# Kernel tuning notes

Measured on AMD Instinct MI355X. Metric: run time of the kernel, lower is better.

The kernel has to match this reference:

```python
import jax, jax.numpy as jnp
import numpy as np

B, T, N, C = 4, 12, 200, 64
ATT = 128      # hard-coded attention_dim in GCN_OPERATION
H = 64         # AdjGen LSTM hidden size
DA = 64        # AdjGen adjacency projection dim
OUT_F = 128    # num_of_out_features
PRED = 12      # predict_length
NFILT = 3      # len(filters) per STSGCM
DATA_LEN = T - 4  # after 2 STSGCL layers


def setup_inputs() -> dict:
    key = jax.random.key(0)
    ks = jax.random.split(key, 16)
    s = 0.05
    f32 = jnp.float32
    return {
        "x": jax.random.normal(ks[0], (B, T, N, C), f32),
        "cur_epi": 5,
        "his_hn": jax.random.normal(ks[1], (B, H), f32),
        "his_cn": jax.random.normal(ks[2], (B, H), f32),
        "Wqkv": jax.random.normal(ks[3], (C, 3 * ATT), f32) * s,
        "bqkv": jnp.zeros((3 * ATT,), f32),
        "Wlin": jax.random.normal(ks[4], (ATT, C), f32) * s,
        "blin": jnp.zeros((C,), f32),
        "Wa": jax.random.normal(ks[5], (C, DA), f32) * s,
        "Wb": jax.random.normal(ks[6], (C, DA), f32) * s,
        "Wx_lstm": jax.random.normal(ks[7], (C, 4 * H), f32) * s,
        "Wh_lstm": jax.random.normal(ks[8], (H, 4 * H), f32) * s,
        "b_lstm": jnp.zeros((4 * H,), f32),
        "temb0": jax.random.normal(ks[9], (1, T, 1, C), f32) * 0.01,
        "temb1": jax.random.normal(ks[10], (1, T - 2, 1, C), f32) * 0.01,
        "semb": jax.random.normal(ks[11], (1, 1, N, C), f32) * 0.01,
        "Wo": jax.random.normal(ks[12], (DATA_LEN * C, OUT_F), f32) * s,
        "bo": jnp.zeros((OUT_F,), f32),
    }


def _forward(x, his_hn, his_cn, Wqkv, bqkv, Wlin, blin, Wa, Wb,
             Wx_lstm, Wh_lstm, b_lstm, temb0, temb1, semb, Wo, bo):
    dt = x.dtype
    att_scale = jnp.sqrt(jnp.asarray(float(ATT), dt))
    adj_scale = jnp.sqrt(jnp.asarray(float(DA), dt))

    def adjgen(xw):
        # xw: (B, nw, M, C). Stand-in for AdjGen (source unavailable):
        # content-dependent learned adjacency over M=3N nodes + one LSTM step.
        node = xw.mean(axis=(0, 1))                                  # (M, C)
        logits = (node @ Wa) @ (node @ Wb).T / adj_scale             # (M, M)
        adj = jax.nn.sigmoid(logits)
        pooled = xw.mean(axis=(1, 2))                                # (B, C)
        gates = pooled @ Wx_lstm + his_hn @ Wh_lstm + b_lstm
        i, f, g, o = jnp.split(gates, 4, axis=-1)
        c_n = jax.nn.sigmoid(f) * his_cn + jax.nn.sigmoid(i) * jnp.tanh(g)
        h_n = jax.nn.sigmoid(o) * jnp.tanh(c_n)
        return adj, logits, h_n, c_n

    def gcn_op(xw, adj):
        # QK^T softmax attention rescaled by adj, renormalized, then AV.
        Bn, nw, M, Cc = xw.shape
        xf = xw.reshape(Bn * nw, M, Cc)
        qkv = xf @ Wqkv + bqkv
        q, k, v = jnp.split(qkv, 3, axis=-1)                          # (BW, M, ATT)
        scores = jnp.einsum('bmd,bnd->bmn', q, k) / att_scale         # (BW, M, M)
        aw = jax.nn.softmax(scores, axis=-1) * adj
        ssum = aw.sum(-1, keepdims=True)
        mask = (ssum > 0).astype(dt)
        w = aw / (ssum + 1e-8) * mask
        out = jnp.einsum('bmn,bnd->bmd', w, jax.nn.relu(v)) @ Wlin + blin
        return out.reshape(Bn, nw, M, -1)

    def stsgcm(xw, Nn):
        cands = []
        cur = xw
        hn = cn = None
        for _ in range(NFILT):
            adj, _logits, hn, cn = adjgen(cur)
            cur = gcn_op(cur, adj)
            Bn, nw, M, F = cur.shape
            # keep only the middle-window copy of the N vertices: [2N:3N]
            cands.append(cur.reshape(Bn * nw, M, F)[:, 2 * Nn:3 * Nn, :])
        out = jnp.max(jnp.stack(cands, axis=0), axis=0)               # (B*nw, N, F)
        return out, hn, cn

    def stsgcl(xw, temb):
        Bn, Tt, Nn, Cc = xw.shape
        xw = xw + temb + semb                                         # position embedding
        nw = Tt - 2
        idx = jnp.arange(nw)[:, None] + jnp.arange(3)[None, :]        # (nw, 3)
        t_all = xw[:, idx].reshape(Bn, nw, 3 * Nn, Cc)
        out, hn, cn = stsgcm(t_all, Nn)
        return out.reshape(Bn, nw, Nn, -1), hn, cn

    h, hn, cn = stsgcl(x, temb0)
    h, hn, cn = stsgcl(h, temb1)
    # OUTPUT layer: (B, T', N, F) -> (B, N, T'*F) -> ReLU(Linear) -> tile PRED times on dim 1
    Bn, Tt, Nn, F = h.shape
    d = h.transpose(0, 2, 1, 3).reshape(Bn, Nn, Tt * F)
    o1 = jax.nn.relu(d @ Wo + bo)                                     # (B, N, OUT_F)
    return jnp.tile(o1, (1, PRED, 1))                                 # (B, PRED*N, OUT_F)


def reference(x, cur_epi, his_hn, his_cn, Wqkv, bqkv, Wlin, blin, Wa, Wb,
              Wx_lstm, Wh_lstm, b_lstm, temb0, temb1, semb, Wo, bo):
    del cur_epi  # annealing schedule of the (unavailable) AdjGen; unused here
    return _forward(x, his_hn, his_cn, Wqkv, bqkv, Wlin, blin, Wa, Wb,
                    Wx_lstm, Wh_lstm, b_lstm, temb0, temb1, semb, Wo, bo)
```

## Files before the change

### kernel.cpp

```cpp
#include <hip/hip_runtime.h>
#include <hip/hip_bf16.h>
#include <math.h>

constexpr int Bc   = 4;
constexpr int Nc   = 200;
constexpr int Cc   = 64;
constexpr int Mc   = 600;
constexpr int ATTc = 128;
constexpr int OUTFc = 128;
constexpr int PREDc = 12;
constexpr int MAXBW = 40;
constexpr int MPAD  = 640;

typedef short short4v __attribute__((ext_vector_type(4)));
typedef short short8 __attribute__((ext_vector_type(8)));
typedef float f32x4  __attribute__((ext_vector_type(4)));

static __device__ __forceinline__ void bsplit(float v, short& h, short& l) {
    __hip_bfloat16 hb = __float2bfloat16(v);
    float hf = __bfloat162float(hb);
    __hip_bfloat16 lb = __float2bfloat16(v - hf);
    h = *(short*)&hb; l = *(short*)&lb;
}

__global__ __launch_bounds__(256)
void embed_window_k(const float* __restrict__ src, const float* __restrict__ temb,
                    const float* __restrict__ semb, float* __restrict__ dst,
                    int Tin, int nw, long total)
{
    long idx = (long)blockIdx.x * 256 + threadIdx.x;
    if (idx >= total) return;
    int c = (int)(idx & 63);
    long r = idx >> 6;
    int n = (int)(r % Nc); r /= Nc;
    int j = (int)(r % 3);  r /= 3;
    int w = (int)(r % nw);
    int b = (int)(r / nw);
    int t = w + j;
    dst[idx] = src[(((long)b * Tin + t) * Nc + n) * Cc + c]
             + temb[t * Cc + c] + semb[n * Cc + c];
}

__global__ __launch_bounds__(256)
void mean_nab_k(const float* __restrict__ cur, const float* __restrict__ Wa,
                const float* __restrict__ Wb,
                ushort* __restrict__ NAH, ushort* __restrict__ NAL,
                ushort* __restrict__ NBH, ushort* __restrict__ NBL, int BW)
{
    __shared__ float Ns[64][17];
    __shared__ float Ws[64][132];
    const int m0 = blockIdx.x * 16;
    const int t = threadIdx.x;
    for (int e = t; e < 1024; e += 256) {
        int r = e >> 4, c4 = (e & 15) << 2;
        *(float4*)&Ws[r][c4]      = *(const float4*)&Wa[r * 64 + c4];
        *(float4*)&Ws[r][64 + c4] = *(const float4*)&Wb[r * 64 + c4];
    }
    {
        int row = t >> 4, c4 = (t & 15) << 2;
        int gm = m0 + row;
        float4 sv = make_float4(0.f, 0.f, 0.f, 0.f);
        if (gm < Mc) {
            for (int bw = 0; bw < BW; bw++) {
                const float4 v = *(const float4*)&cur[((long)bw * Mc + gm) * Cc + c4];
                sv.x += v.x; sv.y += v.y; sv.z += v.z; sv.w += v.w;
            }
        }
        const float inv = 1.f / BW;
        Ns[c4 + 0][row] = sv.x * inv; Ns[c4 + 1][row] = sv.y * inv;
        Ns[c4 + 2][row] = sv.z * inv; Ns[c4 + 3][row] = sv.w * inv;
    }
    __syncthreads();
    const int row = t >> 4, c8 = (t & 15) * 8;
    float acc[8] = {};
    for (int k = 0; k < 64; k++) {
        float a = Ns[k][row];
        float b[8];
        *(float4*)&b[0] = *(const float4*)&Ws[k][c8];
        *(float4*)&b[4] = *(const float4*)&Ws[k][c8 + 4];
#pragma unroll
        for (int j = 0; j < 8; j++) acc[j] += a * b[j];
    }
    int gm = m0 + row;
    if (gm < Mc) {
#pragma unroll
        for (int j = 0; j < 8; j++) {
            int col = c8 + j;
            short h, l;
            bsplit(acc[j], h, l);
            if (col < 64) { NAH[gm * 64 + col] = (ushort)h; NAL[gm * 64 + col] = (ushort)l; }
            else { NBH[gm * 64 + col - 64] = (ushort)h; NBL[gm * 64 + col - 64] = (ushort)l; }
        }
    }
}

__global__ __launch_bounds__(256)
void adjmm_k(const ushort* __restrict__ Ah, const ushort* __restrict__ Al,
             const ushort* __restrict__ Bh, const ushort* __restrict__ Bl,
             float* __restrict__ ADJ)
{
    __shared__ __align__(16) ushort As[2][128][40];
    __shared__ __align__(16) ushort Bs[2][128][40];
    const int m0 = blockIdx.y * 128, n0 = blockIdx.x * 128;
    const int t = threadIdx.x;
    const int lane = t & 63, w = t >> 6;
    const int wm = (w >> 1) * 64, wn = (w & 1) * 64;
    const int lm = lane & 15, lq = lane >> 4;

    f32x4 acc[4][4];
#pragma unroll
    for (int i = 0; i < 4; i++)
#pragma unroll
        for (int j = 0; j < 4; j++)
#pragma unroll
            for (int r = 0; r < 4; r++) acc[i][j][r] = 0.f;

    for (int k0 = 0; k0 < 64; k0 += 32) {
        __syncthreads();
#pragma unroll
        for (int p = 0; p < 2; p++) {
            int e = t + p * 256;
            int row = e >> 2, ks = (e & 3) << 3;
            {
                int gm = m0 + row;
                short8 vh, vl;
#pragma unroll
                for (int q = 0; q < 8; q++) { vh[q] = 0; vl[q] = 0; }
                if (gm < Mc) {
                    vh = *(const short8*)(Ah + (long)gm * 64 + k0 + ks);
                    vl = *(const short8*)(Al + (long)gm * 64 + k0 + ks);
                }
                *(short8*)&As[0][row][ks] = vh;
                *(short8*)&As[1][row][ks] = vl;
            }
            {
                int gn = n0 + row;
                short8 vh, vl;
#pragma unroll
                for (int q = 0; q < 8; q++) { vh[q] = 0; vl[q] = 0; }
                if (gn < Mc) {
                    vh = *(const short8*)(Bh + (long)gn * 64 + k0 + ks);
                    vl = *(const short8*)(Bl + (long)gn * 64 + k0 + ks);
                }
                *(short8*)&Bs[0][row][ks] = vh;
                *(short8*)&Bs[1][row][ks] = vl;
            }
        }
        __syncthreads();

        short8 af[4][2], bf[4][2];
#pragma unroll
        for (int i = 0; i < 4; i++) {
            af[i][0] = *(const short8*)&As[0][wm + i * 16 + lm][lq * 8];
            af[i][1] = *(const short8*)&As[1][wm + i * 16 + lm][lq * 8];
        }
#pragma unroll
        for (int j = 0; j < 4; j++) {
            bf[j][0] = *(const short8*)&Bs[0][wn + j * 16 + lm][lq * 8];
            bf[j][1] = *(const short8*)&Bs[1][wn + j * 16 + lm][lq * 8];
        }
#pragma unroll
        for (int i = 0; i < 4; i++)
#pragma unroll
            for (int j = 0; j < 4; j++) {
                acc[i][j] = __builtin_amdgcn_mfma_f32_16x16x32_bf16(af[i][0], bf[j][0], acc[i][j], 0, 0, 0);
                acc[i][j] = __builtin_amdgcn_mfma_f32_16x16x32_bf16(af[i][0], bf[j][1], acc[i][j], 0, 0, 0);
                acc[i][j] = __builtin_amdgcn_mfma_f32_16x16x32_bf16(af[i][1], bf[j][0], acc[i][j], 0, 0, 0);
            }
    }
#pragma unroll
    for (int i = 0; i < 4; i++) {
        int gmb = m0 + wm + i * 16 + lq * 4;
#pragma unroll
        for (int j = 0; j < 4; j++) {
            int gn = n0 + wn + j * 16 + lm;
            if (gn >= Mc) continue;
#pragma unroll
            for (int r = 0; r < 4; r++) {
                int gm = gmb + r;
                if (gm < Mc)
                    ADJ[(long)gm * Mc + gn] = 1.f / (1.f + __expf(-acc[i][j][r] * 0.125f));
            }
        }
    }
}

__global__ __launch_bounds__(256)
void wqkv_prep_k(const float* __restrict__ Wqkv,
                 ushort* __restrict__ WQH, ushort* __restrict__ WQL)
{
    int i = blockIdx.x * 256 + threadIdx.x;
    if (i >= 384 * 64) return;
    int n = i >> 6, c = i & 63;
    short h, l;
    bsplit(Wqkv[c * 384 + n], h, l);
    WQH[n * 64 + c] = (ushort)h;
    WQL[n * 64 + c] = (ushort)l;
}

__global__ __launch_bounds__(256)
void qkv_mfma_k(const float* __restrict__ CURp,
                const ushort* __restrict__ WQH, const ushort* __restrict__ WQL,
                const float* __restrict__ bias,
                ushort* __restrict__ QH, ushort* __restrict__ QL,
                ushort* __restrict__ KH, ushort* __restrict__ KL,
                ushort* __restrict__ VTH, ushort* __restrict__ VTL)
{
    __shared__ __align__(16) ushort SM[36864];
    ushort* AsH = SM;
    ushort* AsL = SM + 9216;
    ushort* BsH = SM + 18432;
    ushort* BsL = SM + 27648;
    const int bid = blockIdx.x;
    const int xcd = bid & 7, slot = bid >> 3;
    const int z = (slot / 15) * 8 + xcd;
    const int r15 = slot % 15;
    const int which = r15 % 3;
    const int m0 = (r15 / 3) * 128;
    const int nb = which * 128;
    const float* A = CURp + (long)z * Mc * Cc;
    const int t = threadIdx.x;
    const int lane = t & 63, w = t >> 6;
    const int wm = (w >> 1) * 64, wn = (w & 1) * 64;
    const int lm = lane & 15, lq = lane >> 4;

#pragma unroll
    for (int p = 0; p < 8; p++) {
        int e = t + p * 256;
        int row = e >> 4, k4 = (e & 15) * 4;
        int gm = m0 + row;
        float4 v = make_float4(0.f, 0.f, 0.f, 0.f);
        if (gm < Mc) v = *(const float4*)(A + (long)gm * 64 + k4);
        short4v h4, l4;
        short hs, ls;
        bsplit(v.x, hs, ls); h4[0] = hs; l4[0] = ls;
        bsplit(v.y, hs, ls); h4[1] = hs; l4[1] = ls;
        bsplit(v.z, hs, ls); h4[2] = hs; l4[2] = ls;
        bsplit(v.w, hs, ls); h4[3] = hs; l4[3] = ls;
        *(short4v*)(AsH + row * 72 + k4) = h4;
        *(short4v*)(AsL + row * 72 + k4) = l4;
    }
#pragma unroll
    for (int p = 0; p < 4; p++) {
        int e = t + p * 256;
        int row = e >> 3, seg = (e & 7) * 8;
        *(short8*)(BsH + row * 72 + seg) = *(const short8*)(WQH + (long)(nb + row) * 64 + seg);
        *(short8*)(BsL + row * 72 + seg) = *(const short8*)(WQL + (long)(nb + row) * 64 + seg);
    }
    __syncthreads();

    f32x4 acc[4][4];
#pragma unroll
    for (int i = 0; i < 4; i++)
#pragma unroll
        for (int j = 0; j < 4; j++)
#pragma unroll
            for (int r = 0; r < 4; r++) acc[i][j][r] = 0.f;

#pragma unroll
    for (int ks = 0; ks < 2; ks++) {
        short8 af[4][2], bf[4][2];
#pragma unroll
        for (int i = 0; i < 4; i++) {
            af[i][0] = *(const short8*)(AsH + (wm + i * 16 + lm) * 72 + ks * 32 + lq * 8);
            af[i][1] = *(const short8*)(AsL + (wm + i * 16 + lm) * 72 + ks * 32 + lq * 8);
        }
#pragma unroll
        for (int j = 0; j < 4; j++) {
            bf[j][0] = *(const short8*)(BsH + (wn + j * 16 + lm) * 72 + ks * 32 + lq * 8);
            bf[j][1] = *(const short8*)(BsL + (wn + j * 16 + lm) * 72 + ks * 32 + lq * 8);
        }
#pragma unroll
        for (int i = 0; i < 4; i++)
#pragma unroll
            for (int j = 0; j < 4; j++) {
                acc[i][j] = __builtin_amdgcn_mfma_f32_16x16x32_bf16(af[i][0], bf[j][0], acc[i][j], 0, 0, 0);
                acc[i][j] = __builtin_amdgcn_mfma_f32_16x16x32_bf16(af[i][0], bf[j][1], acc[i][j], 0, 0, 0);
                acc[i][j] = __builtin_amdgcn_mfma_f32_16x16x32_bf16(af[i][1], bf[j][0], acc[i][j], 0, 0, 0);
            }
    }
    __syncthreads();

    uint* CP = (uint*)SM;
#pragma unroll
    for (int i = 0; i < 4; i++)
#pragma unroll
        for (int j = 0; j < 4; j++) {
            int col = wn + j * 16 + lm;
            float b = bias[nb + col];
#pragma unroll
            for (int r = 0; r < 4; r++) {
                int row = wm + i * 16 + lq * 4 + r;
                float v = acc[i][j][r] + b;
                if (which == 2) v = fmaxf(v, 0.f);
                short hs, ls;
                bsplit(v, hs, ls);
                CP[row * 132 + col] = ((uint)(ushort)ls << 16) | (uint)(ushort)hs;
            }
        }
    __syncthreads();

    if (which == 2) {
        ushort* vh = VTH + (long)z * ATTc * MPAD;
        ushort* vl = VTL + (long)z * ATTc * MPAD;
#pragma unroll
        for (int p = 0; p < 8; p++) {
            int e = t + p * 256;
            int col = e >> 4, rg = (e & 15) * 8;
            if (m0 + rg < Mc) {
                short8 h8, l8;
#pragma unroll
                for (int q = 0; q < 8; q++) {
                    uint u = CP[(rg + q) * 132 + col];
                    h8[q] = (short)(u & 0xffff);
                    l8[q] = (short)(u >> 16);
                }
                *(short8*)(vh + (long)col * MPAD + m0 + rg) = h8;
                *(short8*)(vl + (long)col * MPAD + m0 + rg) = l8;
            }
        }
    } else {
        ushort* dh = (which == 0 ? QH : KH) + (long)z * Mc * ATTc;
        ushort* dl = (which == 0 ? QL : KL) + (long)z * Mc * ATTc;
#pragma unroll
        for (int p = 0; p < 8; p++) {
            int e = t + p * 256;
            int row = e >> 4, seg = (e & 15) * 8;
            int gm = m0 + row;
            if (gm < Mc) {
                short8 h8, l8;
#pragma unroll
                for (int q = 0; q < 8; q++) {
                    uint u = CP[row * 132 + seg + q];
                    h8[q] = (short)(u & 0xffff);
                    l8[q] = (short)(u >> 16);
                }
                *(short8*)(dh + (long)gm * ATTc + seg) = h8;
                *(short8*)(dl + (long)gm * ATTc + seg) = l8;
            }
        }
    }
}

#define ISSUE_K(Dh, Dl, kc_, g_)                                        \
  _Pragma("unroll")                                                     \
  for (int p = 0; p < 4; p++) {                                         \
    int key = (kc_) + srow0 + 32 * p;                                   \
    short8 vh, vl;                                                      \
    _Pragma("unroll")                                                   \
    for (int q2 = 0; q2 < 8; q2++) { vh[q2] = 0; vl[q2] = 0; }          \
    if (key < Mc) {                                                     \
      vh = *(const short8*)(Khz + (long)key * ATTc + (g_) * 64 + sks);  \
      vl = *(const short8*)(Klz + (long)key * ATTc + (g_) * 64 + sks);  \
    }                                                                   \
    Dh[p] = vh; Dl[p] = vl;                                             \
  }

#define ISSUE_V(Dh, Dl, kc_, g_)                                                   \
  _Pragma("unroll")                                                                \
  for (int p = 0; p < 4; p++) {                                                    \
    int att = srow0 + 32 * p;                                                      \
    Dh[p] = *(const short8*)(Vhz + (long)att * MPAD + (kc_) + (g_) * 64 + sks);    \
    Dl[p] = *(const short8*)(Vlz + (long)att * MPAD + (kc_) + (g_) * 64 + sks);    \
  }

#define WRITE_SB(Dh, Dl)                                                \
  _Pragma("unroll")                                                     \
  for (int p = 0; p < 4; p++) {                                         \
    *(short8*)&SB[0][srow0 + 32 * p][sks] = Dh[p];                      \
    *(short8*)&SB[1][srow0 + 32 * p][sks] = Dl[p];                      \
  }

#define MFMA_QK(base_)                                                   \
  _Pragma("unroll")                                                      \
  for (int kk = 0; kk < 2; kk++) {                                       \
    _Pragma("unroll")                                                    \
    for (int j = 0; j < 8; j++) {                                        \
      short8 bh = *(const short8*)&SB[0][j * 16 + lm][kk * 32 + lq * 8]; \
      short8 bl = *(const short8*)&SB[1][j * 16 + lm][kk * 32 + lq * 8]; \
      sacc[j] = __builtin_amdgcn_mfma_f32_16x16x32_bf16(qh[(base_) + kk], bh, sacc[j], 0, 0, 0); \
      sacc[j] = __builtin_amdgcn_mfma_f32_16x16x32_bf16(qh[(base_) + kk], bl, sacc[j], 0, 0, 0); \
      sacc[j] = __builtin_amdgcn_mfma_f32_16x16x32_bf16(ql[(base_) + kk], bh, sacc[j], 0, 0, 0); \
    }                                                                    \
  }

#define MFMA_PV(g_)                                                      \
  _Pragma("unroll")                                                      \
  for (int kk = 0; kk < 2; kk++) {                                       \
    int po = ((g_) * 64 + kk * 32 + lq * 8) ^ ((lm >> 2) << 3);          \
    short8 ph = *(const short8*)&PH[w][lm][po];                          \
    short8 pl = *(const short8*)&PL[w][lm][po];                          \
    _Pragma("unroll")                                                    \
    for (int j = 0; j < 8; j++) {                                        \
      short8 vh = *(const short8*)&SB[0][j * 16 + lm][kk * 32 + lq * 8]; \
      short8 vl = *(const short8*)&SB[1][j * 16 + lm][kk * 32 + lq * 8]; \
      oacc[j] = __builtin_amdgcn_mfma_f32_16x16x32_bf16(ph, vh, oacc[j], 0, 0, 0); \
      oacc[j] = __builtin_amdgcn_mfma_f32_16x16x32_bf16(ph, vl, oacc[j], 0, 0, 0); \
      oacc[j] = __builtin_amdgcn_mfma_f32_16x16x32_bf16(pl, vh, oacc[j], 0, 0, 0); \
    }                                                                    \
  }

__global__ __launch_bounds__(256, 2)
void attn_k(const ushort* __restrict__ QH, const ushort* __restrict__ QL,
            const ushort* __restrict__ KH, const ushort* __restrict__ KL,
            const ushort* __restrict__ VTH, const ushort* __restrict__ VTL,
            const float* __restrict__ adj, uint* __restrict__ OB, float scale)
{
    __shared__ __align__(16) ushort SB[2][128][72];
    __shared__ __align__(16) ushort PH[4][16][152];
    __shared__ __align__(16) ushort PL[4][16][152];
    const int bid = blockIdx.x;
    const int xcd = bid & 7, slot = bid >> 3;
    const int z = (slot / 10) * 8 + xcd;
    const int m0 = (slot % 10) * 64;
    const int t = threadIdx.x;
    const int lane = t & 63, w = t >> 6;
    const int lm = lane & 15, lq = lane >> 4;
    const int qrow0 = m0 + w * 16;
    const int srow0 = t >> 3;
    const int sks   = (t & 7) << 3;

    const ushort* Qhz = QH + (long)z * Mc * ATTc;
    const ushort* Qlz = QL + (long)z * Mc * ATTc;
    const ushort* Khz = KH + (long)z * Mc * ATTc;
    const ushort* Klz = KL + (long)z * Mc * ATTc;
    const ushort* Vhz = VTH + (long)z * ATTc * MPAD;
    const ushort* Vlz = VTL + (long)z * ATTc * MPAD;

    short8 RAh[4], RAl[4], RBh[4], RBl[4];
    ISSUE_K(RAh, RAl, 0, 0);

    short8 qh[4], ql[4];
    {
        int qr = qrow0 + lm;
        if (qr < Mc) {
            const ushort* qp = Qhz + (long)qr * ATTc;
            const ushort* qp2 = Qlz + (long)qr * ATTc;
#pragma unroll
            for (int ks = 0; ks < 4; ks++) {
                qh[ks] = *(const short8*)(qp + ks * 32 + lq * 8);
                ql[ks] = *(const short8*)(qp2 + ks * 32 + lq * 8);
            }
        } else {
#pragma unroll
            for (int ks = 0; ks < 4; ks++)
#pragma unroll
                for (int q = 0; q < 8; q++) { qh[ks][q] = 0; ql[ks][q] = 0; }
        }
    }

    f32x4 oacc[8];
#pragma unroll
    for (int j = 0; j < 8; j++)
#pragma unroll
        for (int r = 0; r < 4; r++) oacc[j][r] = 0.f;
    float Er[4] = {}, Sr[4] = {};
    float adjv[8][4];

    for (int c = 0; c < 5; c++) {
        const int kc = c * 128;
        f32x4 sacc[8];
#pragma unroll
        for (int j = 0; j < 8; j++)
#pragma unroll
            for (int r = 0; r < 4; r++) sacc[j][r] = 0.f;

        __syncthreads();
        WRITE_SB(RAh, RAl);
        ISSUE_K(RBh, RBl, kc, 1);
#pragma unroll
        for (int j = 0; j < 8; j++) {
            int col = kc + j * 16 + lm;
#pragma unroll
            for (int r = 0; r < 4; r++) {
                int row = qrow0 + lq * 4 + r;
                adjv[j][r] = (col < Mc && row < Mc) ? adj[(long)row * Mc + col] : 0.f;
            }
        }
        __syncthreads();
        MFMA_QK(0);

        __syncthreads();
        WRITE_SB(RBh, RBl);
        ISSUE_V(RAh, RAl, kc, 0);
        __syncthreads();
        MFMA_QK(2);

#pragma unroll
        for (int j = 0; j < 8; j++) {
            int col = kc + j * 16 + lm;
            bool cok = col < Mc;
#pragma unroll
            for (int r = 0; r < 4; r++) {
                float e = cok ? __expf(sacc[j][r] * scale) : 0.f;
                float p = e * adjv[j][r];
                Er[r] += e; Sr[r] += p;
                short hs, ls;
                bsplit(p, hs, ls);
                int cs = (j * 16 + lm) ^ (lq << 3);
                PH[w][lq * 4 + r][cs] = (ushort)hs;
                PL[w][lq * 4 + r][cs] = (ushort)ls;
            }
        }

        __syncthreads();
        WRITE_SB(RAh, RAl);
        ISSUE_V(RBh, RBl, kc, 1);
        __syncthreads();
        MFMA_PV(0);

        __syncthreads();
        WRITE_SB(RBh, RBl);
        if (c < 4) { ISSUE_K(RAh, RAl, kc + 128, 0); }
        __syncthreads();
        MFMA_PV(1);
    }

#pragma unroll
    for (int mk = 1; mk <= 8; mk <<= 1)
#pragma unroll
        for (int r = 0; r < 4; r++) {
            Er[r] += __shfl_xor(Er[r], mk, 64);
            Sr[r] += __shfl_xor(Sr[r], mk, 64);
        }
    float inv[4];
#pragma unroll
    for (int r = 0; r < 4; r++) inv[r] = 1.f / (Sr[r] + 1e-8f * Er[r]);
    uint* Oz = OB + (long)z * Mc * ATTc;
#pragma unroll
    for (int j = 0; j < 8; j++)
#pragma unroll
        for (int r = 0; r < 4; r++) {
            int row = qrow0 + lq * 4 + r;
            if (row < Mc) {
                float v = oacc[j][r] * inv[r];
                short hs, ls;
                bsplit(v, hs, ls);
                Oz[(long)row * ATTc + j * 16 + lm] =
                    ((uint)(ushort)ls << 16) | (uint)(ushort)hs;
            }
        }
}

#undef ISSUE_K
#undef ISSUE_V
#undef WRITE_SB
#undef MFMA_QK
#undef MFMA_PV

__global__ __launch_bounds__(256)
void wlin_prep_k(const float* __restrict__ Wlin,
                 ushort* __restrict__ WTH, ushort* __restrict__ WTL)
{
    int i = blockIdx.x * 256 + threadIdx.x;
    if (i >= 64 * 128) return;
    int c = i >> 7, a = i & 127;
    short h, l;
    bsplit(Wlin[a * 64 + c], h, l);
    WTH[c * 128 + a] = (ushort)h;
    WTL[c * 128 + a] = (ushort)l;
}

__global__ __launch_bounds__(256)
void wlin_k(const uint* __restrict__ OB, const ushort* __restrict__ WTH,
            const ushort* __restrict__ WTL, const float* __restrict__ blin,
            float* __restrict__ CUR, int Mtot)
{
    __shared__ __align__(16) ushort As[2][128][40];
    __shared__ __align__(16) ushort Bs[2][64][136];
    const int m0 = blockIdx.x * 128;
    const int t = threadIdx.x;
    const int lane = t & 63, w = t >> 6;
    const int wm = (w >> 1) * 64, wn = (w & 1) * 32;
    const int lm = lane & 15, lq = lane >> 4;

#pragma unroll
    for (int p = 0; p < 4; p++) {
        int e = t + p * 256;
        int row = e >> 4, seg = (e & 15) << 3;
        *(short8*)&Bs[0][row][seg] = *(const short8*)(WTH + row * 128 + seg);
        *(short8*)&Bs[1][row][seg] = *(const short8*)(WTL + row * 128 + seg);
    }

    f32x4 acc[4][2];
#pragma unroll
    for (int i = 0; i < 4; i++)
#pragma unroll
        for (int j = 0; j < 2; j++)
#pragma unroll
            for (int r = 0; r < 4; r++) acc[i][j][r] = 0.f;

    for (int k0 = 0; k0 < 128; k0 += 32) {
        __syncthreads();
#pragma unroll
        for (int p = 0; p < 2; p++) {
            int e = t + p * 256;
            int row = e >> 2, seg = (e & 3) << 3;
            int gm = m0 + row;
            short8 vh, vl;
#pragma unroll
            for (int q = 0; q < 8; q++) { vh[q] = 0; vl[q] = 0; }
            if (gm < Mtot) {
                const uint4 u0 = *(const uint4*)(OB + (long)gm * 128 + k0 + seg);
                const uint4 u1 = *(const uint4*)(OB + (long)gm * 128 + k0 + seg + 4);
#pragma unroll
                for (int q = 0; q < 4; q++) {
                    uint u = ((const uint*)&u0)[q];
                    vh[q] = (short)(u & 0xffff); vl[q] = (short)(u >> 16);
                }
#pragma unroll
                for (int q = 0; q < 4; q++) {
                    uint u = ((const uint*)&u1)[q];
                    vh[4 + q] = (short)(u & 0xffff); vl[4 + q] = (short)(u >> 16);
                }
            }
            *(short8*)&As[0][row][seg] = vh;
            *(short8*)&As[1][row][seg] = vl;
        }
        __syncthreads();

        short8 af[4][2], bf[2][2];
#pragma unroll
        for (int i = 0; i < 4; i++) {
            af[i][0] = *(const short8*)&As[0][wm + i * 16 + lm][lq * 8];
            af[i][1] = *(const short8*)&As[1][wm + i * 16 + lm][lq * 8];
        }
#pragma unroll
        for (int j = 0; j < 2; j++) {
            bf[j][0] = *(const short8*)&Bs[0][wn + j * 16 + lm][k0 + lq * 8];
            bf[j][1] = *(const short8*)&Bs[1][wn + j * 16 + lm][k0 + lq * 8];
        }
#pragma unroll
        for (int i = 0; i < 4; i++)
#pragma unroll
            for (int j = 0; j < 2; j++) {
                acc[i][j] = __builtin_amdgcn_mfma_f32_16x16x32_bf16(af[i][0], bf[j][0], acc[i][j], 0, 0, 0);
                acc[i][j] = __builtin_amdgcn_mfma_f32_16x16x32_bf16(af[i][0], bf[j][1], acc[i][j], 0, 0, 0);
                acc[i][j] = __builtin_amdgcn_mfma_f32_16x16x32_bf16(af[i][1], bf[j][0], acc[i][j], 0, 0, 0);
            }
    }
#pragma unroll
    for (int i = 0; i < 4; i++) {
        int gmb = m0 + wm + i * 16 + lq * 4;
#pragma unroll
        for (int j = 0; j < 2; j++) {
            int col = wn + j * 16 + lm;
            float b = blin[col];
#pragma unroll
            for (int r = 0; r < 4; r++) {
                int gm = gmb + r;
                if (gm < Mtot) CUR[(long)gm * 64 + col] = acc[i][j][r] + b;
            }
        }
    }
}

__global__ __launch_bounds__(256)
void cand_update_k(const float* __restrict__ cur, float* __restrict__ cand,
                   int bw0, long total, int first)
{
    long idx = (long)blockIdx.x * 256 + threadIdx.x;
    if (idx >= total) return;
    int c = (int)(idx & 63);
    long r = idx >> 6;
    int n = (int)(r % Nc);
    int i = (int)(r / Nc);
    long bw = bw0 + i;
    float v = cur[((bw * Mc) + 2 * Nc + n) * Cc + c];
    long o = ((bw * Nc) + n) * Cc + c;
    cand[o] = first ? v : fmaxf(cand[o], v);
}

__global__ __launch_bounds__(128)
void output_k(const float* __restrict__ h2, const float* __restrict__ Wo,
              const float* __restrict__ bo, float* __restrict__ out)
{
    __shared__ float ds[512];
    int row = blockIdx.x;
    int b = row / Nc, n = row % Nc;
    int t = threadIdx.x;
    for (int e = t; e < 512; e += 128) {
        int tt = e >> 6, c = e & 63;
        ds[e] = h2[(((long)b * 8 + tt) * Nc + n) * Cc + c];
    }
    __syncthreads();
    float acc = bo[t];
    for (int e = 0; e < 512; e++) acc += ds[e] * Wo[e * OUTFc + t];
    acc = fmaxf(acc, 0.f);
    for (int p = 0; p < PREDc; p++)
        out[(((long)b * PREDc + p) * Nc + n) * (long)OUTFc + t] = acc;
}

extern "C" void kernel_launch(void* const* d_in, const int* in_sizes, int n_in,
                              void* d_out, int out_size, void* d_ws, size_t ws_size,
                              hipStream_t stream)
{
    (void)in_sizes; (void)n_in; (void)out_size; (void)ws_size;
    const float* x     = (const float*)d_in[0];
    const float* Wqkv  = (const float*)d_in[4];
    const float* bqkv  = (const float*)d_in[5];
    const float* Wlin  = (const float*)d_in[6];
    const float* blin  = (const float*)d_in[7];
    const float* Wa    = (const float*)d_in[8];
    const float* Wb    = (const float*)d_in[9];
    const float* temb0 = (const float*)d_in[13];
    const float* temb1 = (const float*)d_in[14];
    const float* semb  = (const float*)d_in[15];
    const float* Wo    = (const float*)d_in[16];
    const float* bo    = (const float*)d_in[17];
    float* out = (float*)d_out;

    float* ws   = (float*)d_ws;
    float* CUR  = ws;
    float* ADJ  = CUR + (long)MAXBW * Mc * Cc;
    float* CAND = ADJ + (long)Mc * Mc;
    uint*  OB   = (uint*)(CAND + (long)MAXBW * Nc * Cc);
    float* QHf  = (float*)(OB + (long)MAXBW * Mc * ATTc);
    const long QSZ = (long)MAXBW * Mc * ATTc / 2;
    float* QLf  = QHf + QSZ;
    float* KHf  = QLf + QSZ;
    float* KLf  = KHf + QSZ;
    float* VTHf = KLf + QSZ;
    float* VTLf = VTHf + (long)MAXBW * ATTc * MPAD / 2;
    ushort* NAH = (ushort*)(VTLf + (long)MAXBW * ATTc * MPAD / 2);
    ushort* NAL = NAH + Mc * Cc;
    ushort* NBH = NAL + Mc * Cc;
    ushort* NBL = NBH + Mc * Cc;
    ushort* WTH = NBL + Mc * Cc;
    ushort* WTL = WTH + 64 * 128;
    ushort* WQH = WTL + 64 * 128;
    ushort* WQL = WQH + 384 * 64;

    ushort* QH  = (ushort*)QHf;
    ushort* QL  = (ushort*)QLf;
    ushort* KH  = (ushort*)KHf;
    ushort* KL  = (ushort*)KLf;
    ushort* VTH = (ushort*)VTHf;
    ushort* VTL = (ushort*)VTLf;

    const float inv_sqrt_att = 0.08838834764831845f;

    wlin_prep_k<<<dim3(32), dim3(256), 0, stream>>>(Wlin, WTH, WTL);
    wqkv_prep_k<<<dim3(96), dim3(256), 0, stream>>>(Wqkv, WQH, WQL);

    for (int layer = 0; layer < 2; layer++) {
        int Tin = layer ? 10 : 12;
        int nw  = Tin - 2;
        int BW  = Bc * nw;
        int Mtot = BW * Mc;
        const float* src  = layer ? CAND : x;
        const float* temb = layer ? temb1 : temb0;

        long etotal = (long)BW * Mc * Cc;
        embed_window_k<<<dim3((unsigned)((etotal + 255) / 256)), dim3(256), 0, stream>>>(
            src, temb, semb, CUR, Tin, nw, etotal);

        for (int it = 0; it < 3; it++) {
            mean_nab_k<<<dim3(38), dim3(256), 0, stream>>>(
                CUR, Wa, Wb, NAH, NAL, NBH, NBL, BW);
            adjmm_k<<<dim3(5, 5), dim3(256), 0, stream>>>(
                NAH, NAL, NBH, NBL, ADJ);

            qkv_mfma_k<<<dim3(BW * 15), dim3(256), 0, stream>>>(
                CUR, WQH, WQL, bqkv, QH, QL, KH, KL, VTH, VTL);

            attn_k<<<dim3(BW * 10), dim3(256), 0, stream>>>(
                QH, QL, KH, KL, VTH, VTL, ADJ, OB, inv_sqrt_att);

            wlin_k<<<dim3((Mtot + 127) / 128), dim3(256), 0, stream>>>(
                OB, WTH, WTL, blin, CUR, Mtot);

            long mtot = (long)BW * Nc * Cc;
            cand_update_k<<<dim3((unsigned)((mtot + 255) / 256)), dim3(256), 0, stream>>>(
                CUR, CAND, 0, mtot, it == 0 ? 1 : 0);
        }
    }
    output_k<<<dim3(Bc * Nc), dim3(128), 0, stream>>>(CAND, Wo, bo, out);
}
```

Baseline: 753.0 us.

## Use 32x32 MFMA tiles in attention and fuse candidate max into wlin

Moves the attention kernel from 16x16x32 to 32x32x16 bf16 MFMA instructions. Each wave now owns a 32-query by 64-key/attn quadrant, which cuts LDS operand reads per flop. A shared-memory reduction combines the softmax row sums across the two key-half waves. It also folds the per-iteration candidate max update into the wlin epilogue, removing a separate kernel launch and one re-read of CUR. The trade-offs are higher register pressure from the 16-wide accumulators and an extra block barrier.

```diff
diff --git a/kernel.cpp b/kernel.cpp
--- a/kernel.cpp
+++ b/kernel.cpp
@@ -15,6 +15,7 @@
 typedef short short4v __attribute__((ext_vector_type(4)));
 typedef short short8 __attribute__((ext_vector_type(8)));
 typedef float f32x4  __attribute__((ext_vector_type(4)));
+typedef float f32x16 __attribute__((ext_vector_type(16)));
 
 static __device__ __forceinline__ void bsplit(float v, short& h, short& l) {
     __hip_bfloat16 hb = __float2bfloat16(v);
@@ -371,33 +372,35 @@
     *(short8*)&SB[1][srow0 + 32 * p][sks] = Dl[p];                      \
   }
 
-#define MFMA_QK(base_)                                                   \
-  _Pragma("unroll")                                                      \
-  for (int kk = 0; kk < 2; kk++) {                                       \
-    _Pragma("unroll")                                                    \
-    for (int j = 0; j < 8; j++) {                                        \
-      short8 bh = *(const short8*)&SB[0][j * 16 + lm][kk * 32 + lq * 8]; \
-      short8 bl = *(const short8*)&SB[1][j * 16 + lm][kk * 32 + lq * 8]; \
-      sacc[j] = __builtin_amdgcn_mfma_f32_16x16x32_bf16(qh[(base_) + kk], bh, sacc[j], 0, 0, 0); \
-      sacc[j] = __builtin_amdgcn_mfma_f32_16x16x32_bf16(qh[(base_) + kk], bl, sacc[j], 0, 0, 0); \
-      sacc[j] = __builtin_amdgcn_mfma_f32_16x16x32_bf16(ql[(base_) + kk], bh, sacc[j], 0, 0, 0); \
-    }                                                                    \
+#define MFMA32(a, b, c) __builtin_amdgcn_mfma_f32_32x32x16_bf16(a, b, c, 0, 0, 0)
+
+#define QK_ROUND(g_)                                                       \
+  _Pragma("unroll")                                                        \
+  for (int al = 0; al < 4; al++) {                                         \
+    short8 b0h = *(const short8*)&SB[0][kh64 + l31][al * 16 + lh8];        \
+    short8 b0l = *(const short8*)&SB[1][kh64 + l31][al * 16 + lh8];        \
+    short8 b1h = *(const short8*)&SB[0][kh64 + 32 + l31][al * 16 + lh8];   \
+    short8 b1l = *(const short8*)&SB[1][kh64 + 32 + l31][al * 16 + lh8];   \
+    s0 = MFMA32(qh[(g_) * 4 + al], b0h, s0);                               \
+    s1 = MFMA32(qh[(g_) * 4 + al], b1h, s1);                               \
+    s0 = MFMA32(qh[(g_) * 4 + al], b0l, s0);                               \
+    s1 = MFMA32(qh[(g_) * 4 + al], b1l, s1);                               \
+    s0 = MFMA32(ql[(g_) * 4 + al], b0h, s0);                               \
+    s1 = MFMA32(ql[(g_) * 4 + al], b1h, s1);                               \
   }
 
-#define MFMA_PV(g_)                                                      \
-  _Pragma("unroll")                                                      \
-  for (int kk = 0; kk < 2; kk++) {                                       \
-    int po = ((g_) * 64 + kk * 32 + lq * 8) ^ ((lm >> 2) << 3);          \
-    short8 ph = *(const short8*)&PH[w][lm][po];                          \
-    short8 pl = *(const short8*)&PL[w][lm][po];                          \
-    _Pragma("unroll")                                                    \
-    for (int j = 0; j < 8; j++) {                                        \
-      short8 vh = *(const short8*)&SB[0][j * 16 + lm][kk * 32 + lq * 8]; \
-      short8 vl = *(const short8*)&SB[1][j * 16 + lm][kk * 32 + lq * 8]; \
-      oacc[j] = __builtin_amdgcn_mfma_f32_16x16x32_bf16(ph, vh, oacc[j], 0, 0, 0); \
-      oacc[j] = __builtin_amdgcn_mfma_f32_16x16x32_bf16(ph, vl, oacc[j], 0, 0, 0); \
-      oacc[j] = __builtin_amdgcn_mfma_f32_16x16x32_bf16(pl, vh, oacc[j], 0, 0, 0); \
-    }                                                                    \
+#define PV_ROUND(g_)                                                       \
+  _Pragma("unroll")                                                        \
+  for (int kp = 0; kp < 4; kp++) {                                         \
+    short8 pA = *(const short8*)&PHs[qt32 + l31][(g_) * 64 + kp * 16 + lh8]; \
+    short8 pB = *(const short8*)&PLs[qt32 + l31][(g_) * 64 + kp * 16 + lh8]; \
+    short8 v0h = *(const short8*)&SB[0][kh64 + l31][kp * 16 + lh8];        \
+    short8 v0l = *(const short8*)&SB[1][kh64 + l31][kp * 16 + lh8];        \
+    short8 v1h = *(const short8*)&SB[0][kh64 + 32 + l31][kp * 16 + lh8];   \
+    short8 v1l = *(const short8*)&SB[1][kh64 + 32 + l31][kp * 16 + lh8];   \
+    o0 = MFMA32(pA, v0h, o0); o1 = MFMA32(pA, v1h, o1);                    \
+    o0 = MFMA32(pA, v0l, o0); o1 = MFMA32(pA, v1l, o1);                    \
+    o0 = MFMA32(pB, v0h, o0); o1 = MFMA32(pB, v1h, o1);                    \
   }
 
 __global__ __launch_bounds__(256, 2)
@@ -407,16 +410,19 @@
             const float* __restrict__ adj, uint* __restrict__ OB, float scale)
 {
     __shared__ __align__(16) ushort SB[2][128][72];
-    __shared__ __align__(16) ushort PH[4][16][152];
-    __shared__ __align__(16) ushort PL[4][16][152];
+    __shared__ __align__(16) ushort PHs[64][136];
+    __shared__ __align__(16) ushort PLs[64][136];
+    __shared__ float REDs[2][2][2][16];
+    __shared__ float REDe[2][2][2][16];
     const int bid = blockIdx.x;
     const int xcd = bid & 7, slot = bid >> 3;
     const int z = (slot / 10) * 8 + xcd;
     const int m0 = (slot % 10) * 64;
     const int t = threadIdx.x;
     const int lane = t & 63, w = t >> 6;
-    const int lm = lane & 15, lq = lane >> 4;
-    const int qrow0 = m0 + w * 16;
+    const int l31 = lane & 31, lh = lane >> 5, lh8 = lh * 8;
+    const int qt = w & 1, kh = w >> 1;
+    const int qt32 = qt * 32, kh64 = kh * 64;
     const int srow0 = t >> 3;
     const int sks   = (t & 7) << 3;
 
@@ -430,76 +436,74 @@
     short8 RAh[4], RAl[4], RBh[4], RBl[4];
     ISSUE_K(RAh, RAl, 0, 0);
 
-    short8 qh[4], ql[4];
+    short8 qh[8], ql[8];
     {
-        int qr = qrow0 + lm;
+        int qr = m0 + qt32 + l31;
         if (qr < Mc) {
-            const ushort* qp = Qhz + (long)qr * ATTc;
+            const ushort* qp  = Qhz + (long)qr * ATTc;
             const ushort* qp2 = Qlz + (long)qr * ATTc;
 #pragma unroll
-            for (int ks = 0; ks < 4; ks++) {
-                qh[ks] = *(const short8*)(qp + ks * 32 + lq * 8);
-                ql[ks] = *(const short8*)(qp2 + ks * 32 + lq * 8);
+            for (int a = 0; a < 8; a++) {
+                qh[a] = *(const short8*)(qp + a * 16 + lh8);
+                ql[a] = *(const short8*)(qp2 + a * 16 + lh8);
             }
         } else {
 #pragma unroll
-            for (int ks = 0; ks < 4; ks++)
-#pragma unroll
-                for (int q = 0; q < 8; q++) { qh[ks][q] = 0; ql[ks][q] = 0; }
-        }
-    }
-
-    f32x4 oacc[8];
-#pragma unroll
-    for (int j = 0; j < 8; j++)
-#pragma unroll
-        for (int r = 0; r < 4; r++) oacc[j][r] = 0.f;
-    float Er[4] = {}, Sr[4] = {};
-    float adjv[8][4];
+            for (int a = 0; a < 8; a++)
+#pragma unroll
+                for (int q = 0; q < 8; q++) { qh[a][q] = 0; ql[a][q] = 0; }
+        }
+    }
+
+    f32x16 o0, o1;
+#pragma unroll
+    for (int r = 0; r < 16; r++) { o0[r] = 0.f; o1[r] = 0.f; }
+    float Er[16] = {}, Sr[16] = {};
 
     for (int c = 0; c < 5; c++) {
         const int kc = c * 128;
-        f32x4 sacc[8];
-#pragma unroll
-        for (int j = 0; j < 8; j++)
-#pragma unroll
-            for (int r = 0; r < 4; r++) sacc[j][r] = 0.f;
+        f32x16 s0, s1;
+#pragma unroll
+        for (int r = 0; r < 16; r++) { s0[r] = 0.f; s1[r] = 0.f; }
 
         __syncthreads();
         WRITE_SB(RAh, RAl);
         ISSUE_K(RBh, RBl, kc, 1);
-#pragma unroll
-        for (int j = 0; j < 8; j++) {
-            int col = kc + j * 16 + lm;
-#pragma unroll
-            for (int r = 0; r < 4; r++) {
-                int row = qrow0 + lq * 4 + r;
-                adjv[j][r] = (col < Mc && row < Mc) ? adj[(long)row * Mc + col] : 0.f;
-            }
-        }
-        __syncthreads();
-        MFMA_QK(0);
+        __syncthreads();
+        QK_ROUND(0);
 
         __syncthreads();
         WRITE_SB(RBh, RBl);
         ISSUE_V(RAh, RAl, kc, 0);
         __syncthreads();
-        MFMA_QK(2);
-
-#pragma unroll
-        for (int j = 0; j < 8; j++) {
-            int col = kc + j * 16 + lm;
-            bool cok = col < Mc;
-#pragma unroll
-            for (int r = 0; r < 4; r++) {
-                float e = cok ? __expf(sacc[j][r] * scale) : 0.f;
-                float p = e * adjv[j][r];
-                Er[r] += e; Sr[r] += p;
+        QK_ROUND(1);
+
+        {
+            int c0 = kc + kh64 + l31, c1 = c0 + 32;
+            bool c0ok = c0 < Mc, c1ok = c1 < Mc;
+            float av0[16], av1[16];
+#pragma unroll
+            for (int r = 0; r < 16; r++) {
+                int rl = (r & 3) + 8 * (r >> 2) + 4 * lh;
+                int row = m0 + qt32 + rl;
+                bool rok = row < Mc;
+                av0[r] = (rok && c0ok) ? adj[(long)row * Mc + c0] : 0.f;
+                av1[r] = (rok && c1ok) ? adj[(long)row * Mc + c1] : 0.f;
+            }
+#pragma unroll
+            for (int r = 0; r < 16; r++) {
+                int rl = (r & 3) + 8 * (r >> 2) + 4 * lh;
+                float e0 = c0ok ? __expf(s0[r] * scale) : 0.f;
+                float e1 = c1ok ? __expf(s1[r] * scale) : 0.f;
+                float p0 = e0 * av0[r], p1 = e1 * av1[r];
+                Er[r] += e0 + e1; Sr[r] += p0 + p1;
                 short hs, ls;
-                bsplit(p, hs, ls);
-                int cs = (j * 16 + lm) ^ (lq << 3);
-                PH[w][lq * 4 + r][cs] = (ushort)hs;
-                PL[w][lq * 4 + r][cs] = (ushort)ls;
+                bsplit(p0, hs, ls);
+                PHs[qt32 + rl][kh64 + l31] = (ushort)hs;
+                PLs[qt32 + rl][kh64 + l31] = (ushort)ls;
+                bsplit(p1, hs, ls);
+                PHs[qt32 + rl][kh64 + 32 + l31] = (ushort)hs;
+                PLs[qt32 + rl][kh64 + 32 + l31] = (ushort)ls;
             }
         }
 
@@ -507,46 +511,62 @@
         WRITE_SB(RAh, RAl);
         ISSUE_V(RBh, RBl, kc, 1);
         __syncthreads();
-        MFMA_PV(0);
+        PV_ROUND(0);
 
         __syncthreads();
         WRITE_SB(RBh, RBl);
         if (c < 4) { ISSUE_K(RAh, RAl, kc + 128, 0); }
         __syncthreads();
-        MFMA_PV(1);
-    }
-
-#pragma unroll
-    for (int mk = 1; mk <= 8; mk <<= 1)
-#pragma unroll
-        for (int r = 0; r < 4; r++) {
+        PV_ROUND(1);
+    }
+
+#pragma unroll
+    for (int mk = 1; mk <= 16; mk <<= 1)
+#pragma unroll
+        for (int r = 0; r < 16; r++) {
             Er[r] += __shfl_xor(Er[r], mk, 64);
             Sr[r] += __shfl_xor(Sr[r], mk, 64);
         }
-    float inv[4];
-#pragma unroll
-    for (int r = 0; r < 4; r++) inv[r] = 1.f / (Sr[r] + 1e-8f * Er[r]);
+    if (l31 == 0) {
+#pragma unroll
+        for (int r = 0; r < 16; r++) {
+            REDs[qt][kh][lh][r] = Sr[r];
+            REDe[qt][kh][lh][r] = Er[r];
+        }
+    }
+    __syncthreads();
+    float inv[16];
+#pragma unroll
+    for (int r = 0; r < 16; r++) {
+        float S = REDs[qt][0][lh][r] + REDs[qt][1][lh][r];
+        float E = REDe[qt][0][lh][r] + REDe[qt][1][lh][r];
+        inv[r] = 1.f / (S + 1e-8f * E);
+    }
     uint* Oz = OB + (long)z * Mc * ATTc;
 #pragma unroll
-    for (int j = 0; j < 8; j++)
-#pragma unroll
-        for (int r = 0; r < 4; r++) {
-            int row = qrow0 + lq * 4 + r;
-            if (row < Mc) {
-                float v = oacc[j][r] * inv[r];
-                short hs, ls;
-                bsplit(v, hs, ls);
-                Oz[(long)row * ATTc + j * 16 + lm] =
-                    ((uint)(ushort)ls << 16) | (uint)(ushort)hs;
-            }
-        }
+    for (int r = 0; r < 16; r++) {
+        int rl = (r & 3) + 8 * (r >> 2) + 4 * lh;
+        int row = m0 + qt32 + rl;
+        if (row < Mc) {
+            short hs, ls;
+            float v0 = o0[r] * inv[r];
+            bsplit(v0, hs, ls);
+            Oz[(long)row * ATTc + kh64 + l31] =
+                ((uint)(ushort)ls << 16) | (uint)(ushort)hs;
+            float v1 = o1[r] * inv[r];
+            bsplit(v1, hs, ls);
+            Oz[(long)row * ATTc + kh64 + 32 + l31] =
+                ((uint)(ushort)ls << 16) | (uint)(ushort)hs;
+        }
+    }
 }
 
 #undef ISSUE_K
 #undef ISSUE_V
 #undef WRITE_SB
-#undef MFMA_QK
-#undef MFMA_PV
+#undef QK_ROUND
+#undef PV_ROUND
+#undef MFMA32
 
 __global__ __launch_bounds__(256)
 void wlin_prep_k(const float* __restrict__ Wlin,
@@ -564,7 +584,8 @@
 __global__ __launch_bounds__(256)
 void wlin_k(const uint* __restrict__ OB, const ushort* __restrict__ WTH,
             const ushort* __restrict__ WTL, const float* __restrict__ blin,
-            float* __restrict__ CUR, int Mtot)
+            float* __restrict__ CUR, int Mtot,
+            float* __restrict__ cand, int first)
 {
     __shared__ __align__(16) ushort As[2][128][40];
     __shared__ __align__(16) ushort Bs[2][64][136];
@@ -649,26 +670,19 @@
 #pragma unroll
             for (int r = 0; r < 4; r++) {
                 int gm = gmb + r;
-                if (gm < Mtot) CUR[(long)gm * 64 + col] = acc[i][j][r] + b;
-            }
-        }
-    }
-}
-
-__global__ __launch_bounds__(256)
-void cand_update_k(const float* __restrict__ cur, float* __restrict__ cand,
-                   int bw0, long total, int first)
-{
-    long idx = (long)blockIdx.x * 256 + threadIdx.x;
-    if (idx >= total) return;
-    int c = (int)(idx & 63);
-    long r = idx >> 6;
-    int n = (int)(r % Nc);
-    int i = (int)(r / Nc);
-    long bw = bw0 + i;
-    float v = cur[((bw * Mc) + 2 * Nc + n) * Cc + c];
-    long o = ((bw * Nc) + n) * Cc + c;
-    cand[o] = first ? v : fmaxf(cand[o], v);
+                if (gm < Mtot) {
+                    float v = acc[i][j][r] + b;
+                    CUR[(long)gm * 64 + col] = v;
+                    int bw = gm / Mc;
+                    int m = gm - bw * Mc;
+                    if (m >= 2 * Nc) {
+                        long o = ((long)bw * Nc + (m - 2 * Nc)) * Cc + col;
+                        cand[o] = first ? v : fmaxf(cand[o], v);
+                    }
+                }
+            }
+        }
+    }
 }
 
 __global__ __launch_bounds__(128)
@@ -768,11 +782,7 @@
                 QH, QL, KH, KL, VTH, VTL, ADJ, OB, inv_sqrt_att);
 
             wlin_k<<<dim3((Mtot + 127) / 128), dim3(256), 0, stream>>>(
-                OB, WTH, WTL, blin, CUR, Mtot);
-
-            long mtot = (long)BW * Nc * Cc;
-            cand_update_k<<<dim3((unsigned)((mtot + 255) / 256)), dim3(256), 0, stream>>>(
-                CUR, CAND, 0, mtot, it == 0 ? 1 : 0);
+                OB, WTH, WTL, blin, CUR, Mtot, CAND, it == 0 ? 1 : 0);
         }
     }
     output_k<<<dim3(Bc * Nc), dim3(128), 0, stream>>>(CAND, Wo, bo, out);
```

New measurement: 1.023 ms. 35.8% more time.

## Fuse candidate max-update into wlin epilogue and shrink qkv LDS footprint

Applied to the files above, without the earlier changes.

The separate cand_update kernel is removed, and the running max over the last N nodes is folded into the wlin_k epilogue. This saves one launch and a re-read of CUR per iteration. qkv_mfma_k now reads its weight fragments directly from global memory instead of staging them in LDS. Its epilogue transposes the output in two 64-column halves, which halves shared memory (from 72KB to 36KB) to allow higher occupancy, at the cost of uncached-in-LDS global B loads and an extra barrier pair.

```diff
diff --git a/kernel.cpp b/kernel.cpp
--- a/kernel.cpp
+++ b/kernel.cpp
@@ -206,11 +206,9 @@
                 ushort* __restrict__ KH, ushort* __restrict__ KL,
                 ushort* __restrict__ VTH, ushort* __restrict__ VTL)
 {
-    __shared__ __align__(16) ushort SM[36864];
+    __shared__ __align__(16) ushort SM[18432];
     ushort* AsH = SM;
     ushort* AsL = SM + 9216;
-    ushort* BsH = SM + 18432;
-    ushort* BsL = SM + 27648;
     const int bid = blockIdx.x;
     const int xcd = bid & 7, slot = bid >> 3;
     const int z = (slot / 15) * 8 + xcd;
@@ -240,13 +238,6 @@
         *(short4v*)(AsH + row * 72 + k4) = h4;
         *(short4v*)(AsL + row * 72 + k4) = l4;
     }
-#pragma unroll
-    for (int p = 0; p < 4; p++) {
-        int e = t + p * 256;
-        int row = e >> 3, seg = (e & 7) * 8;
-        *(short8*)(BsH + row * 72 + seg) = *(const short8*)(WQH + (long)(nb + row) * 64 + seg);
-        *(short8*)(BsL + row * 72 + seg) = *(const short8*)(WQL + (long)(nb + row) * 64 + seg);
-    }
     __syncthreads();
 
     f32x4 acc[4][4];
@@ -260,15 +251,16 @@
 #pragma unroll
     for (int ks = 0; ks < 2; ks++) {
         short8 af[4][2], bf[4][2];
+#pragma unroll
+        for (int j = 0; j < 4; j++) {
+            const long brow = nb + wn + j * 16 + lm;
+            bf[j][0] = *(const short8*)(WQH + brow * 64 + ks * 32 + lq * 8);
+            bf[j][1] = *(const short8*)(WQL + brow * 64 + ks * 32 + lq * 8);
+        }
 #pragma unroll
         for (int i = 0; i < 4; i++) {
             af[i][0] = *(const short8*)(AsH + (wm + i * 16 + lm) * 72 + ks * 32 + lq * 8);
             af[i][1] = *(const short8*)(AsL + (wm + i * 16 + lm) * 72 + ks * 32 + lq * 8);
-        }
-#pragma unroll
-        for (int j = 0; j < 4; j++) {
-            bf[j][0] = *(const short8*)(BsH + (wn + j * 16 + lm) * 72 + ks * 32 + lq * 8);
-            bf[j][1] = *(const short8*)(BsL + (wn + j * 16 + lm) * 72 + ks * 32 + lq * 8);
         }
 #pragma unroll
         for (int i = 0; i < 4; i++)
@@ -283,62 +275,70 @@
 
     uint* CP = (uint*)SM;
 #pragma unroll
-    for (int i = 0; i < 4; i++)
-#pragma unroll
-        for (int j = 0; j < 4; j++) {
-            int col = wn + j * 16 + lm;
-            float b = bias[nb + col];
-#pragma unroll
-            for (int r = 0; r < 4; r++) {
-                int row = wm + i * 16 + lq * 4 + r;
-                float v = acc[i][j][r] + b;
-                if (which == 2) v = fmaxf(v, 0.f);
-                short hs, ls;
-                bsplit(v, hs, ls);
-                CP[row * 132 + col] = ((uint)(ushort)ls << 16) | (uint)(ushort)hs;
-            }
-        }
-    __syncthreads();
-
-    if (which == 2) {
-        ushort* vh = VTH + (long)z * ATTc * MPAD;
-        ushort* vl = VTL + (long)z * ATTc * MPAD;
-#pragma unroll
-        for (int p = 0; p < 8; p++) {
-            int e = t + p * 256;
-            int col = e >> 4, rg = (e & 15) * 8;
-            if (m0 + rg < Mc) {
-                short8 h8, l8;
-#pragma unroll
-                for (int q = 0; q < 8; q++) {
-                    uint u = CP[(rg + q) * 132 + col];
-                    h8[q] = (short)(u & 0xffff);
-                    l8[q] = (short)(u >> 16);
+    for (int half = 0; half < 2; half++) {
+        if ((w & 1) == half) {
+#pragma unroll
+            for (int i = 0; i < 4; i++)
+#pragma unroll
+                for (int j = 0; j < 4; j++) {
+                    int col = wn + j * 16 + lm;
+                    int lc  = col - half * 64;
+                    float b = bias[nb + col];
+#pragma unroll
+                    for (int r = 0; r < 4; r++) {
+                        int row = wm + i * 16 + lq * 4 + r;
+                        float v = acc[i][j][r] + b;
+                        if (which == 2) v = fmaxf(v, 0.f);
+                        short hs, ls;
+                        bsplit(v, hs, ls);
+                        CP[row * 66 + lc] = ((uint)(ushort)ls << 16) | (uint)(ushort)hs;
+                    }
                 }
-                *(short8*)(vh + (long)col * MPAD + m0 + rg) = h8;
-                *(short8*)(vl + (long)col * MPAD + m0 + rg) = l8;
-            }
-        }
-    } else {
-        ushort* dh = (which == 0 ? QH : KH) + (long)z * Mc * ATTc;
-        ushort* dl = (which == 0 ? QL : KL) + (long)z * Mc * ATTc;
-#pragma unroll
-        for (int p = 0; p < 8; p++) {
-            int e = t + p * 256;
-            int row = e >> 4, seg = (e & 15) * 8;
-            int gm = m0 + row;
-            if (gm < Mc) {
-                short8 h8, l8;
-#pragma unroll
-                for (int q = 0; q < 8; q++) {
-                    uint u = CP[row * 132 + seg + q];
-                    h8[q] = (short)(u & 0xffff);
-                    l8[q] = (short)(u >> 16);
+        }
+        __syncthreads();
+
+        if (which == 2) {
+            ushort* vh = VTH + (long)z * ATTc * MPAD;
+            ushort* vl = VTL + (long)z * ATTc * MPAD;
+#pragma unroll
+            for (int p = 0; p < 4; p++) {
+                int e = t + p * 256;
+                int col = e >> 4, rg = (e & 15) * 8;
+                if (m0 + rg < Mc) {
+                    short8 h8, l8;
+#pragma unroll
+                    for (int q = 0; q < 8; q++) {
+                        uint u = CP[(rg + q) * 66 + col];
+                        h8[q] = (short)(u & 0xffff);
+                        l8[q] = (short)(u >> 16);
+                    }
+                    int gcol = half * 64 + col;
+                    *(short8*)(vh + (long)gcol * MPAD + m0 + rg) = h8;
+                    *(short8*)(vl + (long)gcol * MPAD + m0 + rg) = l8;
                 }
-                *(short8*)(dh + (long)gm * ATTc + seg) = h8;
-                *(short8*)(dl + (long)gm * ATTc + seg) = l8;
-            }
-        }
+            }
+        } else {
+            ushort* dh = (which == 0 ? QH : KH) + (long)z * Mc * ATTc;
+            ushort* dl = (which == 0 ? QL : KL) + (long)z * Mc * ATTc;
+#pragma unroll
+            for (int p = 0; p < 4; p++) {
+                int e = t + p * 256;
+                int row = e >> 3, seg = (e & 7) * 8;
+                int gm = m0 + row;
+                if (gm < Mc) {
+                    short8 h8, l8;
+#pragma unroll
+                    for (int q = 0; q < 8; q++) {
+                        uint u = CP[row * 66 + seg + q];
+                        h8[q] = (short)(u & 0xffff);
+                        l8[q] = (short)(u >> 16);
+                    }
+                    *(short8*)(dh + (long)gm * ATTc + half * 64 + seg) = h8;
+                    *(short8*)(dl + (long)gm * ATTc + half * 64 + seg) = l8;
+                }
+            }
+        }
+        __syncthreads();
     }
 }
 
@@ -564,7 +564,8 @@
 __global__ __launch_bounds__(256)
 void wlin_k(const uint* __restrict__ OB, const ushort* __restrict__ WTH,
             const ushort* __restrict__ WTL, const float* __restrict__ blin,
-            float* __restrict__ CUR, int Mtot)
+            float* __restrict__ CUR, int Mtot,
+            float* __restrict__ cand, int first)
 {
     __shared__ __align__(16) ushort As[2][128][40];
     __shared__ __align__(16) ushort Bs[2][64][136];
@@ -649,26 +650,19 @@
 #pragma unroll
             for (int r = 0; r < 4; r++) {
                 int gm = gmb + r;
-                if (gm < Mtot) CUR[(long)gm * 64 + col] = acc[i][j][r] + b;
-            }
-        }
-    }
-}
-
-__global__ __launch_bounds__(256)
-void cand_update_k(const float* __restrict__ cur, float* __restrict__ cand,
-                   int bw0, long total, int first)
-{
-    long idx = (long)blockIdx.x * 256 + threadIdx.x;
-    if (idx >= total) return;
-    int c = (int)(idx & 63);
-    long r = idx >> 6;
-    int n = (int)(r % Nc);
-    int i = (int)(r / Nc);
-    long bw = bw0 + i;
-    float v = cur[((bw * Mc) + 2 * Nc + n) * Cc + c];
-    long o = ((bw * Nc) + n) * Cc + c;
-    cand[o] = first ? v : fmaxf(cand[o], v);
+                if (gm < Mtot) {
+                    float v = acc[i][j][r] + b;
+                    CUR[(long)gm * 64 + col] = v;
+                    int bw = gm / Mc;
+                    int m = gm - bw * Mc;
+                    if (m >= 2 * Nc) {
+                        long o = ((long)bw * Nc + (m - 2 * Nc)) * Cc + col;
+                        cand[o] = first ? v : fmaxf(cand[o], v);
+                    }
+                }
+            }
+        }
+    }
 }
 
 __global__ __launch_bounds__(128)
@@ -768,11 +762,7 @@
                 QH, QL, KH, KL, VTH, VTL, ADJ, OB, inv_sqrt_att);
 
             wlin_k<<<dim3((Mtot + 127) / 128), dim3(256), 0, stream>>>(
-                OB, WTH, WTL, blin, CUR, Mtot);
-
-            long mtot = (long)BW * Nc * Cc;
-            cand_update_k<<<dim3((unsigned)((mtot + 255) / 256)), dim3(256), 0, stream>>>(
-                CUR, CAND, 0, mtot, it == 0 ? 1 : 0);
+                OB, WTH, WTL, blin, CUR, Mtot, CAND, it == 0 ? 1 : 0);
         }
     }
     output_k<<<dim3(Bc * Nc), dim3(128), 0, stream>>>(CAND, Wo, bo, out);
```

Result: slower. 798.0 us (+6.0%).
